# Kernel tuning notes

Measured on AMD Instinct MI355X. Metric: run time of the kernel, lower is better.

The kernel has to match this reference:

```python
import jax, jax.numpy as jnp
import numpy as np
import math

N_PTS = 262144
STEP_LENGTH = math.sqrt(3.0) / 1024.0  # step_length = sqrt(3)/steps


def pos_enc(x):
    # classic NeRF frequency encoding: identity + sin/cos at 10 octaves -> 3 + 3*2*10 = 63
    freqs = 2.0 ** jnp.arange(10, dtype=x.dtype)            # [10]
    xb = x[..., :, None] * freqs                            # [N,3,10]
    xb = xb.reshape(x.shape[0], -1)                         # [N,30]
    return jnp.concatenate([x, jnp.sin(xb), jnp.cos(xb)], axis=-1)  # [N,63]


def dir_enc(u):
    # 26-dim frequency encoding of (dir+1)/2 (color head input 283 = 256 + 26 + 1).
    # 13 sin/cos pairs: per-channel octaves 2^0..2^4, truncated to 13 frequencies.
    freqs = 2.0 ** jnp.arange(5, dtype=u.dtype)             # [5]
    z = (u[..., :, None] * freqs).reshape(u.shape[0], -1)[:, :13]  # [N,13]
    return jnp.concatenate([jnp.sin(z), jnp.cos(z)], axis=-1)      # [N,26]


def linear(x, w, b):
    return x @ w.T + b


def setup_inputs() -> dict:
    key = jax.random.key(0)
    ks = jax.random.split(key, 16)
    s = 0.05
    inp = {
        "position": jax.random.uniform(ks[0], (N_PTS, 3), dtype=jnp.float32),
        "direction": jax.random.uniform(ks[1], (N_PTS, 3), dtype=jnp.float32, minval=-1.0, maxval=1.0),
        "w1_in": jax.random.normal(ks[2], (256, 63), jnp.float32) * s,
        "b1_in": jnp.zeros((256,), jnp.float32),
        "w1_h": jax.random.normal(ks[3], (3, 256, 256), jnp.float32) * s,
        "b1_h": jnp.zeros((3, 256), jnp.float32),
        "w2_in": jax.random.normal(ks[4], (256, 319), jnp.float32) * s,
        "b2_in": jnp.zeros((256,), jnp.float32),
        "w2_h": jax.random.normal(ks[5], (3, 256, 256), jnp.float32) * s,
        "b2_h": jnp.zeros((3, 256), jnp.float32),
        # sigma head Linear(256,1)
        "w_sigma": jax.random.normal(ks[6], (1, 256), jnp.float32) * s,
        "b_sigma": jnp.zeros((1,), jnp.float32),
        # color head Linear(283,128) -> ReLU -> Linear(128,3)
        "w_c1": jax.random.normal(ks[7], (128, 283), jnp.float32) * s,
        "b_c1": jnp.zeros((128,), jnp.float32),
        "w_c2": jax.random.normal(ks[8], (3, 128), jnp.float32) * s,
        "b_c2": jnp.zeros((3,), jnp.float32),
    }
    return inp


def reference(position, direction,
              w1_in, b1_in, w1_h, b1_h,
              w2_in, b2_in, w2_h, b2_h,
              w_sigma, b_sigma, w_c1, b_c1, w_c2, b_c2):
    pe = pos_enc(position)                                  # [N,63]
    h = jax.nn.relu(linear(pe, w1_in, b1_in))               # [N,256]
    for i in range(3):
        h = jax.nn.relu(linear(h, w1_h[i], b1_h[i]))
    g = jax.nn.relu(linear(jnp.concatenate([h, pe], axis=-1), w2_in, b2_in))  # [N,256]
    for i in range(3):
        g = jax.nn.relu(linear(g, w2_h[i], b2_h[i]))
    sigma_raw = linear(g, w_sigma, b_sigma)                 # [N,1]
    # get_alpha: 1 - exp(-relu(sigma) * step_length)
    alphas = 1.0 - jnp.exp(-jax.nn.relu(sigma_raw) * STEP_LENGTH)             # [N,1]
    # get_rgb: shares base features; concat [256 | 26 | 1] = 283
    de = dir_enc((direction + 1.0) * 0.5)                   # [N,26]
    feats = jnp.concatenate([g, de, sigma_raw], axis=-1)    # [N,283]
    rgb = jax.nn.sigmoid(linear(jax.nn.relu(linear(feats, w_c1, b_c1)), w_c2, b_c2))  # [N,3]
    return (rgb, alphas)
```

## Files before the change

kernel.cpp:

```cpp
#include <hip/hip_runtime.h>
#include <hip/hip_bf16.h>

#define N_PTS 262144
#define STEP_LEN 0.0016914558667664818f

using f32x4 = __attribute__((ext_vector_type(4))) float;
using s8 = __attribute__((ext_vector_type(8))) short;

__device__ __forceinline__ float bf2f(short s) {
    union { unsigned int u; float f; } v;
    v.u = ((unsigned int)(unsigned short)s) << 16;
    return v.f;
}
__device__ __forceinline__ short f2bf(float f) {
    __hip_bfloat16 h = __float2bfloat16(f);
    return *reinterpret_cast<short*>(&h);
}

#define OFF_W1    0
#define OFF_L1H0  16384
#define OFF_W2    212992
#define OFF_L2H0  294912
#define OFF_C1G   491520
#define OFF_C1DE  524288
#define OFF_WSIG  528384
#define OFF_WC2   528640
#define WS_ELEMS  532480

__device__ __forceinline__ float hid_val(const float* __restrict__ W, int e) {
    int j = e & 7, lane = (e >> 3) & 63, nt = (e >> 9) & 15, ks = e >> 13;
    int n = nt * 16 + (lane & 15), hi = lane >> 4;
    int f = ks * 32 + ((j >> 2) << 4) + hi * 4 + (j & 3);
    return W[n * 256 + f];
}

__global__ void prep_weights(const float* __restrict__ w1_in,
                             const float* __restrict__ w1_h,
                             const float* __restrict__ w2_in,
                             const float* __restrict__ w2_h,
                             const float* __restrict__ w_c1,
                             const float* __restrict__ w_sigma,
                             const float* __restrict__ w_c2,
                             __hip_bfloat16* __restrict__ ws) {
    int i = blockIdx.x * blockDim.x + threadIdx.x;
    if (i >= WS_ELEMS) return;
    float v;
    if (i < OFF_L1H0) {
        int e = i;
        int j = e & 7, lane = (e >> 3) & 63, nt = (e >> 9) & 15, ks = e >> 13;
        int n = nt * 16 + (lane & 15), hi = lane >> 4;
        int f = ks * 32 + hi * 8 + j;
        v = (f < 63) ? w1_in[n * 63 + f] : 0.f;
    } else if (i < OFF_W2) {
        int e = i - OFF_L1H0; int sub = e >> 16; e &= 65535;
        v = hid_val(w1_h + sub * 65536, e);
    } else if (i < OFF_L2H0) {
        int e = i - OFF_W2;
        int j = e & 7, lane = (e >> 3) & 63, nt = (e >> 9) & 15, ks = e >> 13;
        int n = nt * 16 + (lane & 15), hi = lane >> 4;
        if (ks < 8) {
            int f = ks * 32 + ((j >> 2) << 4) + hi * 4 + (j & 3);
            v = w2_in[n * 319 + f];
        } else {
            int pf = (ks - 8) * 32 + hi * 8 + j;
            v = (pf < 63) ? w2_in[n * 319 + 256 + pf] : 0.f;
        }
    } else if (i < OFF_C1G) {
        int e = i - OFF_L2H0; int sub = e >> 16; e &= 65535;
        v = hid_val(w2_h + sub * 65536, e);
    } else if (i < OFF_C1DE) {
        int e = i - OFF_C1G;
        int j = e & 7, lane = (e >> 3) & 63, nt = (e >> 9) & 7, ks = e >> 12;
        int n = nt * 16 + (lane & 15), hi = lane >> 4;
        int f = ks * 32 + ((j >> 2) << 4) + hi * 4 + (j & 3);
        v = w_c1[n * 283 + f];
    } else if (i < OFF_WSIG) {
        int e = i - OFF_C1DE;
        int j = e & 7, lane = (e >> 3) & 63, nt = (e >> 9) & 7;
        int n = nt * 16 + (lane & 15), hi = lane >> 4;
        int k = 256 + hi * 8 + j;
        v = (k < 283) ? w_c1[n * 283 + k] : 0.f;
    } else if (i < OFF_WC2) {
        int e = i - OFF_WSIG;
        int j = e & 7, hi = (e >> 3) & 3, ks = e >> 5;
        int f = ks * 32 + ((j >> 2) << 4) + hi * 4 + (j & 3);
        v = w_sigma[f];
    } else if (i < 529024) {
        int e = i - OFF_WC2;
        int j = e & 7, hi = (e >> 3) & 3, ks = (e >> 5) & 3, ch = e >> 7;
        int f = ks * 32 + ((j >> 2) << 4) + hi * 4 + (j & 3);
        v = w_c2[ch * 128 + f];
    } else {
        v = 0.f;
    }
    ws[i] = __float2bfloat16(v);
}

__device__ __forceinline__ float enc3(int f, float x0, float x1, float x2) {
    if (f < 3) return (f == 0) ? x0 : ((f == 1) ? x1 : x2);
    if (f < 33) {
        int q = f - 3; int c = q / 10, o = q % 10;
        float xc = (c == 0) ? x0 : ((c == 1) ? x1 : x2);
        return __sinf(xc * (float)(1 << o));
    }
    if (f < 63) {
        int q = f - 33; int c = q / 10, o = q % 10;
        float xc = (c == 0) ? x0 : ((c == 1) ? x1 : x2);
        return __cosf(xc * (float)(1 << o));
    }
    return 0.f;
}

#define MFMA16 __builtin_amdgcn_mfma_f32_16x16x32_bf16

#define STAGE4(BYTEOFF, DBUF) do { \
    const char* _src = wsB + (long)(BYTEOFF) + wid * 4096 + lane * 16; \
    char* _dst = (DBUF) + wid * 4096; \
    __builtin_amdgcn_global_load_lds((const unsigned int*)(_src),        (unsigned int*)(_dst),        16, 0, 0); \
    __builtin_amdgcn_global_load_lds((const unsigned int*)(_src + 1024), (unsigned int*)(_dst + 1024), 16, 0, 0); \
    __builtin_amdgcn_global_load_lds((const unsigned int*)(_src + 2048), (unsigned int*)(_dst + 2048), 16, 0, 0); \
    __builtin_amdgcn_global_load_lds((const unsigned int*)(_src + 3072), (unsigned int*)(_dst + 3072), 16, 0, 0); \
} while (0)

#define WKSTEP(RDBUF, STGOFF, WRBUF, A0, A1, FIRSTV) do { \
    STAGE4(STGOFF, WRBUF); \
    __builtin_amdgcn_s_setprio(1); \
    _Pragma("unroll") \
    for (int nt = 0; nt < 16; ++nt) { \
        const s8 w = *(const s8*)((RDBUF) + nt * 1024 + lane * 16); \
        acc[nt][0] = MFMA16(w, (A0), (FIRSTV) ? Z : acc[nt][0], 0, 0, 0); \
        acc[nt][1] = MFMA16(w, (A1), (FIRSTV) ? Z : acc[nt][1], 0, 0, 0); \
    } \
    __builtin_amdgcn_s_setprio(0); \
} while (0)

#define KBAR4 do { asm volatile("s_waitcnt vmcnt(4)" ::: "memory"); \
                   __builtin_amdgcn_s_barrier(); } while (0)
#define KBAR0 do { asm volatile("s_waitcnt vmcnt(0)" ::: "memory"); \
                   __builtin_amdgcn_s_barrier(); } while (0)

#define CONVERTL(BOFF) do { \
    _Pragma("unroll") \
    for (int nt = 0; nt < 16; ++nt) { \
        const f32x4 b4 = *(const f32x4*)(biasL + (((BOFF) + nt * 16 + hi4) << 2)); \
        _Pragma("unroll") \
        for (int r = 0; r < 4; ++r) { \
            actA[nt >> 1][((nt & 1) << 2) | r] = f2bf(fmaxf(acc[nt][0][r] + b4[r], 0.f)); \
            actB[nt >> 1][((nt & 1) << 2) | r] = f2bf(fmaxf(acc[nt][1][r] + b4[r], 0.f)); \
        } } } while (0)

#define CKSTEP(RDBUF, KS, FIRSTV) do { \
    __builtin_amdgcn_s_setprio(1); \
    _Pragma("unroll") \
    for (int nt = 0; nt < 8; ++nt) { \
        const s8 w = *(const s8*)((RDBUF) + nt * 1024 + lane * 16); \
        acc[nt][0] = MFMA16(w, actA[KS], (FIRSTV) ? Z : acc[nt][0], 0, 0, 0); \
        acc[nt][1] = MFMA16(w, actB[KS], (FIRSTV) ? Z : acc[nt][1], 0, 0, 0); \
    } \
    _Pragma("unroll") \
    for (int nt = 0; nt < 8; ++nt) { \
        const s8 w = *(const s8*)((RDBUF) + 8192 + nt * 1024 + lane * 16); \
        acc[nt][0] = MFMA16(w, actA[(KS) + 1], acc[nt][0], 0, 0, 0); \
        acc[nt][1] = MFMA16(w, actB[(KS) + 1], acc[nt][1], 0, 0, 0); \
    } \
    __builtin_amdgcn_s_setprio(0); \
} while (0)

__global__ __launch_bounds__(256, 2) void nerf_fused(
    const float* __restrict__ pos, const float* __restrict__ dir,
    const __hip_bfloat16* __restrict__ ws,
    const float* __restrict__ b1_in, const float* __restrict__ b1_h,
    const float* __restrict__ b2_in, const float* __restrict__ b2_h,
    const float* __restrict__ b_sigma, const float* __restrict__ b_c1,
    const float* __restrict__ b_c2,
    float* __restrict__ out) {

    __shared__ __align__(16) char Lds[74240];
    char* const S0 = Lds;
    char* const S1 = Lds + 16384;
    char* const S2 = Lds + 32768;
    char* const S3 = Lds + 49152;
    char* const biasL = Lds + 65536;

    const int t = threadIdx.x;
    const int lane = t & 63;
    const int wid = t >> 6;
    const int hi = lane >> 4;
    const int col = lane & 15;
    const int hi4 = hi * 4;
    const int row0 = blockIdx.x * 128;
    const int gA = row0 + wid * 32 + col;
    const int gB = gA + 16;
    const char* wsB = (const char*)ws;

    for (int i = t; i < 2176; i += 256) {
        float v;
        if (i < 256) v = b1_in[i];
        else if (i < 1024) v = b1_h[i - 256];
        else if (i < 1280) v = b2_in[i - 1024];
        else if (i < 2048) v = b2_h[i - 1280];
        else v = b_c1[i - 2048];
        *(float*)(biasL + i * 4) = v;
    }

    s8 peA0, peA1, peB0, peB1;
    {
        float xa0 = pos[gA*3], xa1 = pos[gA*3+1], xa2 = pos[gA*3+2];
        float xb0 = pos[gB*3], xb1 = pos[gB*3+1], xb2 = pos[gB*3+2];
#pragma unroll
        for (int j = 0; j < 8; ++j) {
            int f0 = hi * 8 + j, f1 = 32 + hi * 8 + j;
            peA0[j] = f2bf(enc3(f0, xa0, xa1, xa2));
            peA1[j] = f2bf(enc3(f1, xa0, xa1, xa2));
            peB0[j] = f2bf(enc3(f0, xb0, xb1, xb2));
            peB1[j] = f2bf(enc3(f1, xb0, xb1, xb2));
        }
    }

    f32x4 acc[16][2];
    s8 actA[8], actB[8];
    const f32x4 Z = {0.f, 0.f, 0.f, 0.f};

    STAGE4(0L, S0);
    STAGE4(16384L, S1);
    asm volatile("s_waitcnt vmcnt(4) lgkmcnt(0)" ::: "memory");
    __builtin_amdgcn_s_barrier();

    WKSTEP(S0, 2L*16384, S2, peA0, peB0, 1); KBAR4;
    WKSTEP(S1, 3L*16384, S3, peA1, peB1, 0); CONVERTL(0); KBAR4;

#pragma unroll 1
    for (int l = 0; l < 3; ++l) {
        const long lb = 65536L + (long)l * 131072;
        const int bo = 256 + (l << 8);
        WKSTEP(S2, lb,            S0, actA[0], actB[0], 1); KBAR4;
        WKSTEP(S3, lb + 16384,    S1, actA[1], actB[1], 0); KBAR4;
        WKSTEP(S0, lb + 2*16384,  S2, actA[2], actB[2], 0); KBAR4;
        WKSTEP(S1, lb + 3*16384,  S3, actA[3], actB[3], 0); KBAR4;
        WKSTEP(S2, lb + 4*16384,  S0, actA[4], actB[4], 0); KBAR4;
        WKSTEP(S3, lb + 5*16384,  S1, actA[5], actB[5], 0); KBAR4;
        WKSTEP(S0, lb + 6*16384,  S2, actA[6], actB[6], 0); KBAR4;
        WKSTEP(S1, lb + 7*16384,  S3, actA[7], actB[7], 0); CONVERTL(bo); KBAR4;
    }

    WKSTEP(S2, 28L*16384, S0, actA[0], actB[0], 1); KBAR4;
    WKSTEP(S3, 29L*16384, S1, actA[1], actB[1], 0); KBAR4;
    WKSTEP(S0, 30L*16384, S2, actA[2], actB[2], 0); KBAR4;
    WKSTEP(S1, 31L*16384, S3, actA[3], actB[3], 0); KBAR4;
    WKSTEP(S2, 32L*16384, S0, actA[4], actB[4], 0); KBAR4;
    WKSTEP(S3, 33L*16384, S1, actA[5], actB[5], 0); KBAR4;
    WKSTEP(S0, 34L*16384, S2, actA[6], actB[6], 0); KBAR4;
    WKSTEP(S1, 35L*16384, S3, actA[7], actB[7], 0); KBAR4;
    WKSTEP(S2, 36L*16384, S0, peA0,    peB0,    0); KBAR4;
    WKSTEP(S3, 37L*16384, S1, peA1,    peB1,    0); CONVERTL(1024); KBAR4;

#pragma unroll 1
    for (int l = 0; l < 3; ++l) {
        const long lb = (long)(38 + (l << 3)) * 16384;
        const int bo = 1280 + (l << 8);
        WKSTEP(S0, lb,            S2, actA[0], actB[0], 1); KBAR4;
        WKSTEP(S1, lb + 16384,    S3, actA[1], actB[1], 0); KBAR4;
        WKSTEP(S2, lb + 2*16384,  S0, actA[2], actB[2], 0); KBAR4;
        WKSTEP(S3, lb + 3*16384,  S1, actA[3], actB[3], 0); KBAR4;
        WKSTEP(S0, lb + 4*16384,  S2, actA[4], actB[4], 0); KBAR4;
        WKSTEP(S1, lb + 5*16384,  S3, actA[5], actB[5], 0); KBAR4;
        WKSTEP(S2, lb + 6*16384,  S0, actA[6], actB[6], 0); KBAR4;
        WKSTEP(S3, lb + 7*16384,  S1, actA[7], actB[7], 0); CONVERTL(bo); KBAR4;
    }

    float alphaA, alphaB, srA, srB;
    {
        float sA = 0.f, sB = 0.f;
#pragma unroll
        for (int ks = 0; ks < 8; ++ks) {
            const s8 wv = *(const s8*)(wsB + (OFF_WSIG + ks * 32 + hi * 8) * 2);
#pragma unroll
            for (int j = 0; j < 8; ++j) {
                sA += bf2f(actA[ks][j]) * bf2f(wv[j]);
                sB += bf2f(actB[ks][j]) * bf2f(wv[j]);
            }
        }
        sA += __shfl_xor(sA, 16); sA += __shfl_xor(sA, 32);
        sB += __shfl_xor(sB, 16); sB += __shfl_xor(sB, 32);
        srA = sA + b_sigma[0]; srB = sB + b_sigma[0];
        alphaA = 1.f - __expf(-fmaxf(srA, 0.f) * STEP_LEN);
        alphaB = 1.f - __expf(-fmaxf(srB, 0.f) * STEP_LEN);
    }

    s8 deA, deB;
    {
        float uA0 = (dir[gA*3+0] + 1.f) * 0.5f;
        float uA1 = (dir[gA*3+1] + 1.f) * 0.5f;
        float uA2 = (dir[gA*3+2] + 1.f) * 0.5f;
        float uB0 = (dir[gB*3+0] + 1.f) * 0.5f;
        float uB1 = (dir[gB*3+1] + 1.f) * 0.5f;
        float uB2 = (dir[gB*3+2] + 1.f) * 0.5f;
#pragma unroll
        for (int j = 0; j < 8; ++j) {
            int d = hi * 8 + j;
            float vA, vB;
            if (d < 13) {
                int c = d / 5, o = d % 5; float s = (float)(1 << o);
                vA = __sinf(((c == 0) ? uA0 : (c == 1) ? uA1 : uA2) * s);
                vB = __sinf(((c == 0) ? uB0 : (c == 1) ? uB1 : uB2) * s);
            } else if (d < 26) {
                int q = d - 13; int c = q / 5, o = q % 5; float s = (float)(1 << o);
                vA = __cosf(((c == 0) ? uA0 : (c == 1) ? uA1 : uA2) * s);
                vB = __cosf(((c == 0) ? uB0 : (c == 1) ? uB1 : uB2) * s);
            } else if (d == 26) {
                vA = srA; vB = srB;
            } else {
                vA = 0.f; vB = 0.f;
            }
            deA[j] = f2bf(vA); deB[j] = f2bf(vB);
        }
    }

    STAGE4(62L*16384, S2); CKSTEP(S0, 0, 1); KBAR4;
    STAGE4(63L*16384, S3); CKSTEP(S1, 2, 0); KBAR4;
    STAGE4(64L*16384, S0); CKSTEP(S2, 4, 0); KBAR4;
    CKSTEP(S3, 6, 0); KBAR0;
    {
        __builtin_amdgcn_s_setprio(1);
#pragma unroll
        for (int nt = 0; nt < 8; ++nt) {
            const s8 w = *(const s8*)(S0 + nt * 1024 + lane * 16);
            acc[nt][0] = MFMA16(w, deA, acc[nt][0], 0, 0, 0);
            acc[nt][1] = MFMA16(w, deB, acc[nt][1], 0, 0, 0);
        }
        __builtin_amdgcn_s_setprio(0);
    }

    s8 c1A[4], c1B[4];
#pragma unroll
    for (int nt = 0; nt < 8; ++nt) {
        const f32x4 b4 = *(const f32x4*)(biasL + ((2048 + nt * 16 + hi4) << 2));
#pragma unroll
        for (int r = 0; r < 4; ++r) {
            c1A[nt >> 1][((nt & 1) << 2) | r] = f2bf(fmaxf(acc[nt][0][r] + b4[r], 0.f));
            c1B[nt >> 1][((nt & 1) << 2) | r] = f2bf(fmaxf(acc[nt][1][r] + b4[r], 0.f));
        }
    }

#pragma unroll
    for (int ch = 0; ch < 3; ++ch) {
        float rA = 0.f, rB = 0.f;
#pragma unroll
        for (int ks = 0; ks < 4; ++ks) {
            const s8 wv = *(const s8*)(wsB + (OFF_WC2 + (ch * 4 + ks) * 32 + hi * 8) * 2);
#pragma unroll
            for (int j = 0; j < 8; ++j) {
                rA += bf2f(c1A[ks][j]) * bf2f(wv[j]);
                rB += bf2f(c1B[ks][j]) * bf2f(wv[j]);
            }
        }
        rA += __shfl_xor(rA, 16); rA += __shfl_xor(rA, 32);
        rB += __shfl_xor(rB, 16); rB += __shfl_xor(rB, 32);
        if (hi == 0) {
            out[gA * 3 + ch] = 1.f / (1.f + __expf(-(rA + b_c2[ch])));
            out[gB * 3 + ch] = 1.f / (1.f + __expf(-(rB + b_c2[ch])));
        }
    }
    if (hi == 0) {
        out[3 * N_PTS + gA] = alphaA;
        out[3 * N_PTS + gB] = alphaB;
    }
}

extern "C" void kernel_launch(void* const* d_in, const int* in_sizes, int n_in,
                              void* d_out, int out_size, void* d_ws, size_t ws_size,
                              hipStream_t stream) {
    const float* position = (const float*)d_in[0];
    const float* direction = (const float*)d_in[1];
    const float* w1_in = (const float*)d_in[2];
    const float* b1_in = (const float*)d_in[3];
    const float* w1_h  = (const float*)d_in[4];
    const float* b1_h  = (const float*)d_in[5];
    const float* w2_in = (const float*)d_in[6];
    const float* b2_in = (const float*)d_in[7];
    const float* w2_h  = (const float*)d_in[8];
    const float* b2_h  = (const float*)d_in[9];
    const float* w_sigma = (const float*)d_in[10];
    const float* b_sigma = (const float*)d_in[11];
    const float* w_c1  = (const float*)d_in[12];
    const float* b_c1  = (const float*)d_in[13];
    const float* w_c2  = (const float*)d_in[14];
    const float* b_c2  = (const float*)d_in[15];
    float* out = (float*)d_out;
    __hip_bfloat16* ws = (__hip_bfloat16*)d_ws;

    prep_weights<<<(WS_ELEMS + 255) / 256, 256, 0, stream>>>(
        w1_in, w1_h, w2_in, w2_h, w_c1, w_sigma, w_c2, ws);

    nerf_fused<<<N_PTS / 128, 256, 0, stream>>>(
        position, direction, ws,
        b1_in, b1_h, b2_in, b2_h,
        b_sigma, b_c1, b_c2, out);
}
```

Measured before the change: 240.3 us.

## Double per-wave row tile to 64 points to halve weight traffic per point

Each wave now processes four 16-row subtiles (64 points) instead of two, so every weight fragment read from LDS feeds four MFMAs. Blocks cover 256 points and the grid is halved. Accumulators grow to 16x4 f32x4, so launch bounds drop to 1 block per CU and the positional encoding is recomputed instead of kept live. The intent is to cut weight staging and LDS reads per point, at the cost of lower occupancy and heavy register pressure that may cause spills.

```diff
diff --git a/kernel.cpp b/kernel.cpp
--- a/kernel.cpp
+++ b/kernel.cpp
@@ -122,14 +122,28 @@
     __builtin_amdgcn_global_load_lds((const unsigned int*)(_src + 3072), (unsigned int*)(_dst + 3072), 16, 0, 0); \
 } while (0)
 
-#define WKSTEP(RDBUF, STGOFF, WRBUF, A0, A1, FIRSTV) do { \
+#define WKSTEP_A(RDBUF, STGOFF, WRBUF, KS, FIRSTV) do { \
     STAGE4(STGOFF, WRBUF); \
     __builtin_amdgcn_s_setprio(1); \
     _Pragma("unroll") \
     for (int nt = 0; nt < 16; ++nt) { \
         const s8 w = *(const s8*)((RDBUF) + nt * 1024 + lane * 16); \
-        acc[nt][0] = MFMA16(w, (A0), (FIRSTV) ? Z : acc[nt][0], 0, 0, 0); \
-        acc[nt][1] = MFMA16(w, (A1), (FIRSTV) ? Z : acc[nt][1], 0, 0, 0); \
+        _Pragma("unroll") \
+        for (int s = 0; s < 4; ++s) \
+            acc[nt][s] = MFMA16(w, act[KS][s], (FIRSTV) ? Z : acc[nt][s], 0, 0, 0); \
+    } \
+    __builtin_amdgcn_s_setprio(0); \
+} while (0)
+
+#define WKSTEP_P(RDBUF, STGOFF, WRBUF, PEV, FIRSTV) do { \
+    STAGE4(STGOFF, WRBUF); \
+    __builtin_amdgcn_s_setprio(1); \
+    _Pragma("unroll") \
+    for (int nt = 0; nt < 16; ++nt) { \
+        const s8 w = *(const s8*)((RDBUF) + nt * 1024 + lane * 16); \
+        _Pragma("unroll") \
+        for (int s = 0; s < 4; ++s) \
+            acc[nt][s] = MFMA16(w, PEV[s], (FIRSTV) ? Z : acc[nt][s], 0, 0, 0); \
     } \
     __builtin_amdgcn_s_setprio(0); \
 } while (0)
@@ -144,9 +158,10 @@
     for (int nt = 0; nt < 16; ++nt) { \
         const f32x4 b4 = *(const f32x4*)(biasL + (((BOFF) + nt * 16 + hi4) << 2)); \
         _Pragma("unroll") \
-        for (int r = 0; r < 4; ++r) { \
-            actA[nt >> 1][((nt & 1) << 2) | r] = f2bf(fmaxf(acc[nt][0][r] + b4[r], 0.f)); \
-            actB[nt >> 1][((nt & 1) << 2) | r] = f2bf(fmaxf(acc[nt][1][r] + b4[r], 0.f)); \
+        for (int s = 0; s < 4; ++s) { \
+            _Pragma("unroll") \
+            for (int r = 0; r < 4; ++r) \
+                act[nt >> 1][s][((nt & 1) << 2) | r] = f2bf(fmaxf(acc[nt][s][r] + b4[r], 0.f)); \
         } } } while (0)
 
 #define CKSTEP(RDBUF, KS, FIRSTV) do { \
@@ -154,19 +169,21 @@
     _Pragma("unroll") \
     for (int nt = 0; nt < 8; ++nt) { \
         const s8 w = *(const s8*)((RDBUF) + nt * 1024 + lane * 16); \
-        acc[nt][0] = MFMA16(w, actA[KS], (FIRSTV) ? Z : acc[nt][0], 0, 0, 0); \
-        acc[nt][1] = MFMA16(w, actB[KS], (FIRSTV) ? Z : acc[nt][1], 0, 0, 0); \
+        _Pragma("unroll") \
+        for (int s = 0; s < 4; ++s) \
+            acc[nt][s] = MFMA16(w, act[KS][s], (FIRSTV) ? Z : acc[nt][s], 0, 0, 0); \
     } \
     _Pragma("unroll") \
     for (int nt = 0; nt < 8; ++nt) { \
         const s8 w = *(const s8*)((RDBUF) + 8192 + nt * 1024 + lane * 16); \
-        acc[nt][0] = MFMA16(w, actA[(KS) + 1], acc[nt][0], 0, 0, 0); \
-        acc[nt][1] = MFMA16(w, actB[(KS) + 1], acc[nt][1], 0, 0, 0); \
+        _Pragma("unroll") \
+        for (int s = 0; s < 4; ++s) \
+            acc[nt][s] = MFMA16(w, act[(KS) + 1][s], acc[nt][s], 0, 0, 0); \
     } \
     __builtin_amdgcn_s_setprio(0); \
 } while (0)
 
-__global__ __launch_bounds__(256, 2) void nerf_fused(
+__global__ __launch_bounds__(256, 1) void nerf_fused(
     const float* __restrict__ pos, const float* __restrict__ dir,
     const __hip_bfloat16* __restrict__ ws,
     const float* __restrict__ b1_in, const float* __restrict__ b1_h,
@@ -188,9 +205,7 @@
     const int hi = lane >> 4;
     const int col = lane & 15;
     const int hi4 = hi * 4;
-    const int row0 = blockIdx.x * 128;
-    const int gA = row0 + wid * 32 + col;
-    const int gB = gA + 16;
+    const int base = blockIdx.x * 256 + wid * 64 + col;
     const char* wsB = (const char*)ws;
 
     for (int i = t; i < 2176; i += 256) {
@@ -203,22 +218,23 @@
         *(float*)(biasL + i * 4) = v;
     }
 
-    s8 peA0, peA1, peB0, peB1;
-    {
-        float xa0 = pos[gA*3], xa1 = pos[gA*3+1], xa2 = pos[gA*3+2];
-        float xb0 = pos[gB*3], xb1 = pos[gB*3+1], xb2 = pos[gB*3+2];
-#pragma unroll
-        for (int j = 0; j < 8; ++j) {
-            int f0 = hi * 8 + j, f1 = 32 + hi * 8 + j;
-            peA0[j] = f2bf(enc3(f0, xa0, xa1, xa2));
-            peA1[j] = f2bf(enc3(f1, xa0, xa1, xa2));
-            peB0[j] = f2bf(enc3(f0, xb0, xb1, xb2));
-            peB1[j] = f2bf(enc3(f1, xb0, xb1, xb2));
-        }
-    }
-
-    f32x4 acc[16][2];
-    s8 actA[8], actB[8];
+    s8 pe0[4], pe1[4];
+    auto make_pe = [&]() {
+#pragma unroll
+        for (int s = 0; s < 4; ++s) {
+            int g = base + s * 16;
+            float x0 = pos[g*3], x1 = pos[g*3+1], x2 = pos[g*3+2];
+#pragma unroll
+            for (int j = 0; j < 8; ++j) {
+                pe0[s][j] = f2bf(enc3(hi * 8 + j, x0, x1, x2));
+                pe1[s][j] = f2bf(enc3(32 + hi * 8 + j, x0, x1, x2));
+            }
+        }
+    };
+    make_pe();
+
+    f32x4 acc[16][4];
+    s8 act[8][4];
     const f32x4 Z = {0.f, 0.f, 0.f, 0.f};
 
     STAGE4(0L, S0);
@@ -226,93 +242,95 @@
     asm volatile("s_waitcnt vmcnt(4) lgkmcnt(0)" ::: "memory");
     __builtin_amdgcn_s_barrier();
 
-    WKSTEP(S0, 2L*16384, S2, peA0, peB0, 1); KBAR4;
-    WKSTEP(S1, 3L*16384, S3, peA1, peB1, 0); CONVERTL(0); KBAR4;
+    WKSTEP_P(S0, 2L*16384, S2, pe0, 1); KBAR4;
+    WKSTEP_P(S1, 3L*16384, S3, pe1, 0); CONVERTL(0); KBAR4;
 
 #pragma unroll 1
     for (int l = 0; l < 3; ++l) {
         const long lb = 65536L + (long)l * 131072;
         const int bo = 256 + (l << 8);
-        WKSTEP(S2, lb,            S0, actA[0], actB[0], 1); KBAR4;
-        WKSTEP(S3, lb + 16384,    S1, actA[1], actB[1], 0); KBAR4;
-        WKSTEP(S0, lb + 2*16384,  S2, actA[2], actB[2], 0); KBAR4;
-        WKSTEP(S1, lb + 3*16384,  S3, actA[3], actB[3], 0); KBAR4;
-        WKSTEP(S2, lb + 4*16384,  S0, actA[4], actB[4], 0); KBAR4;
-        WKSTEP(S3, lb + 5*16384,  S1, actA[5], actB[5], 0); KBAR4;
-        WKSTEP(S0, lb + 6*16384,  S2, actA[6], actB[6], 0); KBAR4;
-        WKSTEP(S1, lb + 7*16384,  S3, actA[7], actB[7], 0); CONVERTL(bo); KBAR4;
-    }
-
-    WKSTEP(S2, 28L*16384, S0, actA[0], actB[0], 1); KBAR4;
-    WKSTEP(S3, 29L*16384, S1, actA[1], actB[1], 0); KBAR4;
-    WKSTEP(S0, 30L*16384, S2, actA[2], actB[2], 0); KBAR4;
-    WKSTEP(S1, 31L*16384, S3, actA[3], actB[3], 0); KBAR4;
-    WKSTEP(S2, 32L*16384, S0, actA[4], actB[4], 0); KBAR4;
-    WKSTEP(S3, 33L*16384, S1, actA[5], actB[5], 0); KBAR4;
-    WKSTEP(S0, 34L*16384, S2, actA[6], actB[6], 0); KBAR4;
-    WKSTEP(S1, 35L*16384, S3, actA[7], actB[7], 0); KBAR4;
-    WKSTEP(S2, 36L*16384, S0, peA0,    peB0,    0); KBAR4;
-    WKSTEP(S3, 37L*16384, S1, peA1,    peB1,    0); CONVERTL(1024); KBAR4;
+        WKSTEP_A(S2, lb,            S0, 0, 1); KBAR4;
+        WKSTEP_A(S3, lb + 16384,    S1, 1, 0); KBAR4;
+        WKSTEP_A(S0, lb + 2*16384,  S2, 2, 0); KBAR4;
+        WKSTEP_A(S1, lb + 3*16384,  S3, 3, 0); KBAR4;
+        WKSTEP_A(S2, lb + 4*16384,  S0, 4, 0); KBAR4;
+        WKSTEP_A(S3, lb + 5*16384,  S1, 5, 0); KBAR4;
+        WKSTEP_A(S0, lb + 6*16384,  S2, 6, 0); KBAR4;
+        WKSTEP_A(S1, lb + 7*16384,  S3, 7, 0); CONVERTL(bo); KBAR4;
+    }
+
+    make_pe();
+
+    WKSTEP_A(S2, 28L*16384, S0, 0, 1); KBAR4;
+    WKSTEP_A(S3, 29L*16384, S1, 1, 0); KBAR4;
+    WKSTEP_A(S0, 30L*16384, S2, 2, 0); KBAR4;
+    WKSTEP_A(S1, 31L*16384, S3, 3, 0); KBAR4;
+    WKSTEP_A(S2, 32L*16384, S0, 4, 0); KBAR4;
+    WKSTEP_A(S3, 33L*16384, S1, 5, 0); KBAR4;
+    WKSTEP_A(S0, 34L*16384, S2, 6, 0); KBAR4;
+    WKSTEP_A(S1, 35L*16384, S3, 7, 0); KBAR4;
+    WKSTEP_P(S2, 36L*16384, S0, pe0, 0); KBAR4;
+    WKSTEP_P(S3, 37L*16384, S1, pe1, 0); CONVERTL(1024); KBAR4;
 
 #pragma unroll 1
     for (int l = 0; l < 3; ++l) {
         const long lb = (long)(38 + (l << 3)) * 16384;
         const int bo = 1280 + (l << 8);
-        WKSTEP(S0, lb,            S2, actA[0], actB[0], 1); KBAR4;
-        WKSTEP(S1, lb + 16384,    S3, actA[1], actB[1], 0); KBAR4;
-        WKSTEP(S2, lb + 2*16384,  S0, actA[2], actB[2], 0); KBAR4;
-        WKSTEP(S3, lb + 3*16384,  S1, actA[3], actB[3], 0); KBAR4;
-        WKSTEP(S0, lb + 4*16384,  S2, actA[4], actB[4], 0); KBAR4;
-        WKSTEP(S1, lb + 5*16384,  S3, actA[5], actB[5], 0); KBAR4;
-        WKSTEP(S2, lb + 6*16384,  S0, actA[6], actB[6], 0); KBAR4;
-        WKSTEP(S3, lb + 7*16384,  S1, actA[7], actB[7], 0); CONVERTL(bo); KBAR4;
-    }
-
-    float alphaA, alphaB, srA, srB;
+        WKSTEP_A(S0, lb,            S2, 0, 1); KBAR4;
+        WKSTEP_A(S1, lb + 16384,    S3, 1, 0); KBAR4;
+        WKSTEP_A(S2, lb + 2*16384,  S0, 2, 0); KBAR4;
+        WKSTEP_A(S3, lb + 3*16384,  S1, 3, 0); KBAR4;
+        WKSTEP_A(S0, lb + 4*16384,  S2, 4, 0); KBAR4;
+        WKSTEP_A(S1, lb + 5*16384,  S3, 5, 0); KBAR4;
+        WKSTEP_A(S2, lb + 6*16384,  S0, 6, 0); KBAR4;
+        WKSTEP_A(S3, lb + 7*16384,  S1, 7, 0); CONVERTL(bo); KBAR4;
+    }
+
+    float sr[4], alpha[4];
     {
-        float sA = 0.f, sB = 0.f;
+        float sm[4] = {0.f, 0.f, 0.f, 0.f};
 #pragma unroll
         for (int ks = 0; ks < 8; ++ks) {
             const s8 wv = *(const s8*)(wsB + (OFF_WSIG + ks * 32 + hi * 8) * 2);
 #pragma unroll
-            for (int j = 0; j < 8; ++j) {
-                sA += bf2f(actA[ks][j]) * bf2f(wv[j]);
-                sB += bf2f(actB[ks][j]) * bf2f(wv[j]);
+            for (int s = 0; s < 4; ++s) {
+#pragma unroll
+                for (int j = 0; j < 8; ++j)
+                    sm[s] += bf2f(act[ks][s][j]) * bf2f(wv[j]);
             }
         }
-        sA += __shfl_xor(sA, 16); sA += __shfl_xor(sA, 32);
-        sB += __shfl_xor(sB, 16); sB += __shfl_xor(sB, 32);
-        srA = sA + b_sigma[0]; srB = sB + b_sigma[0];
-        alphaA = 1.f - __expf(-fmaxf(srA, 0.f) * STEP_LEN);
-        alphaB = 1.f - __expf(-fmaxf(srB, 0.f) * STEP_LEN);
-    }
-
-    s8 deA, deB;
-    {
-        float uA0 = (dir[gA*3+0] + 1.f) * 0.5f;
-        float uA1 = (dir[gA*3+1] + 1.f) * 0.5f;
-        float uA2 = (dir[gA*3+2] + 1.f) * 0.5f;
-        float uB0 = (dir[gB*3+0] + 1.f) * 0.5f;
-        float uB1 = (dir[gB*3+1] + 1.f) * 0.5f;
-        float uB2 = (dir[gB*3+2] + 1.f) * 0.5f;
+#pragma unroll
+        for (int s = 0; s < 4; ++s) {
+            sm[s] += __shfl_xor(sm[s], 16);
+            sm[s] += __shfl_xor(sm[s], 32);
+            sr[s] = sm[s] + b_sigma[0];
+            alpha[s] = 1.f - __expf(-fmaxf(sr[s], 0.f) * STEP_LEN);
+        }
+    }
+
+    s8 de[4];
+#pragma unroll
+    for (int s = 0; s < 4; ++s) {
+        int g = base + s * 16;
+        float u0 = (dir[g*3+0] + 1.f) * 0.5f;
+        float u1 = (dir[g*3+1] + 1.f) * 0.5f;
+        float u2 = (dir[g*3+2] + 1.f) * 0.5f;
 #pragma unroll
         for (int j = 0; j < 8; ++j) {
             int d = hi * 8 + j;
-            float vA, vB;
+            float v;
             if (d < 13) {
-                int c = d / 5, o = d % 5; float s = (float)(1 << o);
-                vA = __sinf(((c == 0) ? uA0 : (c == 1) ? uA1 : uA2) * s);
-                vB = __sinf(((c == 0) ? uB0 : (c == 1) ? uB1 : uB2) * s);
+                int c = d / 5, o = d % 5;
+                v = __sinf(((c == 0) ? u0 : (c == 1) ? u1 : u2) * (float)(1 << o));
             } else if (d < 26) {
-                int q = d - 13; int c = q / 5, o = q % 5; float s = (float)(1 << o);
-                vA = __cosf(((c == 0) ? uA0 : (c == 1) ? uA1 : uA2) * s);
-                vB = __cosf(((c == 0) ? uB0 : (c == 1) ? uB1 : uB2) * s);
+                int q = d - 13; int c = q / 5, o = q % 5;
+                v = __cosf(((c == 0) ? u0 : (c == 1) ? u1 : u2) * (float)(1 << o));
             } else if (d == 26) {
-                vA = srA; vB = srB;
+                v = sr[s];
             } else {
-                vA = 0.f; vB = 0.f;
+                v = 0.f;
             }
-            deA[j] = f2bf(vA); deB[j] = f2bf(vB);
+            de[s][j] = f2bf(v);
         }
     }
 
@@ -325,45 +343,50 @@
 #pragma unroll
         for (int nt = 0; nt < 8; ++nt) {
             const s8 w = *(const s8*)(S0 + nt * 1024 + lane * 16);
-            acc[nt][0] = MFMA16(w, deA, acc[nt][0], 0, 0, 0);
-            acc[nt][1] = MFMA16(w, deB, acc[nt][1], 0, 0, 0);
+#pragma unroll
+            for (int s = 0; s < 4; ++s)
+                acc[nt][s] = MFMA16(w, de[s], acc[nt][s], 0, 0, 0);
         }
         __builtin_amdgcn_s_setprio(0);
     }
 
-    s8 c1A[4], c1B[4];
+    s8 c1[4][4];
 #pragma unroll
     for (int nt = 0; nt < 8; ++nt) {
         const f32x4 b4 = *(const f32x4*)(biasL + ((2048 + nt * 16 + hi4) << 2));
 #pragma unroll
-        for (int r = 0; r < 4; ++r) {
-            c1A[nt >> 1][((nt & 1) << 2) | r] = f2bf(fmaxf(acc[nt][0][r] + b4[r], 0.f));
-            c1B[nt >> 1][((nt & 1) << 2) | r] = f2bf(fmaxf(acc[nt][1][r] + b4[r], 0.f));
+        for (int s = 0; s < 4; ++s) {
+#pragma unroll
+            for (int r = 0; r < 4; ++r)
+                c1[nt >> 1][s][((nt & 1) << 2) | r] = f2bf(fmaxf(acc[nt][s][r] + b4[r], 0.f));
         }
     }
 
 #pragma unroll
     for (int ch = 0; ch < 3; ++ch) {
-        float rA = 0.f, rB = 0.f;
+        float rr[4] = {0.f, 0.f, 0.f, 0.f};
 #pragma unroll
         for (int ks = 0; ks < 4; ++ks) {
             const s8 wv = *(const s8*)(wsB + (OFF_WC2 + (ch * 4 + ks) * 32 + hi * 8) * 2);
 #pragma unroll
-            for (int j = 0; j < 8; ++j) {
-                rA += bf2f(c1A[ks][j]) * bf2f(wv[j]);
-                rB += bf2f(c1B[ks][j]) * bf2f(wv[j]);
+            for (int s = 0; s < 4; ++s) {
+#pragma unroll
+                for (int j = 0; j < 8; ++j)
+                    rr[s] += bf2f(c1[ks][s][j]) * bf2f(wv[j]);
             }
         }
-        rA += __shfl_xor(rA, 16); rA += __shfl_xor(rA, 32);
-        rB += __shfl_xor(rB, 16); rB += __shfl_xor(rB, 32);
-        if (hi == 0) {
-            out[gA * 3 + ch] = 1.f / (1.f + __expf(-(rA + b_c2[ch])));
-            out[gB * 3 + ch] = 1.f / (1.f + __expf(-(rB + b_c2[ch])));
+#pragma unroll
+        for (int s = 0; s < 4; ++s) {
+            rr[s] += __shfl_xor(rr[s], 16);
+            rr[s] += __shfl_xor(rr[s], 32);
+            if (hi == 0)
+                out[(base + s * 16) * 3 + ch] = 1.f / (1.f + __expf(-(rr[s] + b_c2[ch])));
         }
     }
     if (hi == 0) {
-        out[3 * N_PTS + gA] = alphaA;
-        out[3 * N_PTS + gB] = alphaB;
+#pragma unroll
+        for (int s = 0; s < 4; ++s)
+            out[3 * N_PTS + base + s * 16] = alpha[s];
     }
 }
 
@@ -392,7 +415,7 @@
     prep_weights<<<(WS_ELEMS + 255) / 256, 256, 0, stream>>>(
         w1_in, w1_h, w2_in, w2_h, w_c1, w_sigma, w_c2, ws);
 
-    nerf_fused<<<N_PTS / 128, 256, 0, stream>>>(
+    nerf_fused<<<N_PTS / 256, 256, 0, stream>>>(
         position, direction, ws,
         b1_in, b1_h, b2_in, b2_h,
         b_sigma, b_c1, b_c2, out);
```

Measured after the change: 401.1 us. 66.9% more time.

## Stage three quarters of weight tiles via LDS, load last quarter directly to registers

Applied to the files above, without the earlier changes.

Each 16 KB weight chunk is now split so that 12 KB is staged into LDS with global_load_lds and the remaining 4 KB is read by each wave straight from global memory into registers for the last four output tiles. This shrinks the LDS footprint from about 74 KB to 58 KB, which could allow more blocks per CU and reduces LDS traffic. Positional encoding is now computed on demand into a single register pair instead of being held live throughout, lowering register pressure. The trade-off is redundant per-wave global (L2) reads of the direct-loaded portion and more outstanding vector memory operations that must complete before use.

```diff
diff --git a/kernel.cpp b/kernel.cpp
--- a/kernel.cpp
+++ b/kernel.cpp
@@ -113,28 +113,103 @@
 
 #define MFMA16 __builtin_amdgcn_mfma_f32_16x16x32_bf16
 
-#define STAGE4(BYTEOFF, DBUF) do { \
-    const char* _src = wsB + (long)(BYTEOFF) + wid * 4096 + lane * 16; \
-    char* _dst = (DBUF) + wid * 4096; \
-    __builtin_amdgcn_global_load_lds((const unsigned int*)(_src),        (unsigned int*)(_dst),        16, 0, 0); \
-    __builtin_amdgcn_global_load_lds((const unsigned int*)(_src + 1024), (unsigned int*)(_dst + 1024), 16, 0, 0); \
-    __builtin_amdgcn_global_load_lds((const unsigned int*)(_src + 2048), (unsigned int*)(_dst + 2048), 16, 0, 0); \
-    __builtin_amdgcn_global_load_lds((const unsigned int*)(_src + 3072), (unsigned int*)(_dst + 3072), 16, 0, 0); \
+#define GLL(SRC, DST) __builtin_amdgcn_global_load_lds( \
+    (const unsigned int*)(SRC), (unsigned int*)(DST), 16, 0, 0)
+
+#define STAGE3(BYTEOFF, DBUF) do { \
+    const char* _src = wsB + (long)(BYTEOFF) + wid * 3072 + lane * 16; \
+    char* _dst = (DBUF) + wid * 3072; \
+    GLL(_src, _dst); \
+    GLL(_src + 1024, _dst + 1024); \
+    GLL(_src + 2048, _dst + 2048); \
 } while (0)
 
-#define WKSTEP(RDBUF, STGOFF, WRBUF, A0, A1, FIRSTV) do { \
-    STAGE4(STGOFF, WRBUF); \
+#define DLOAD(CUROFF) \
+    const char* _dp = wsB + (long)(CUROFF) + 12288 + lane * 16; \
+    const s8 d0 = *(const s8*)(_dp); \
+    const s8 d1 = *(const s8*)(_dp + 1024); \
+    const s8 d2 = *(const s8*)(_dp + 2048); \
+    const s8 d3 = *(const s8*)(_dp + 3072); \
+    __builtin_amdgcn_sched_barrier(0)
+
+#define WK12_A(RDBUF, CUROFF, STGOFF, WRBUF, KS, FIRSTV) do { \
+    DLOAD(CUROFF); \
+    STAGE3(STGOFF, WRBUF); \
     __builtin_amdgcn_s_setprio(1); \
     _Pragma("unroll") \
-    for (int nt = 0; nt < 16; ++nt) { \
+    for (int nt = 0; nt < 12; ++nt) { \
         const s8 w = *(const s8*)((RDBUF) + nt * 1024 + lane * 16); \
-        acc[nt][0] = MFMA16(w, (A0), (FIRSTV) ? Z : acc[nt][0], 0, 0, 0); \
-        acc[nt][1] = MFMA16(w, (A1), (FIRSTV) ? Z : acc[nt][1], 0, 0, 0); \
+        acc[nt][0] = MFMA16(w, act[KS][0], (FIRSTV) ? Z : acc[nt][0], 0, 0, 0); \
+        acc[nt][1] = MFMA16(w, act[KS][1], (FIRSTV) ? Z : acc[nt][1], 0, 0, 0); \
     } \
+    acc[12][0] = MFMA16(d0, act[KS][0], (FIRSTV) ? Z : acc[12][0], 0, 0, 0); \
+    acc[12][1] = MFMA16(d0, act[KS][1], (FIRSTV) ? Z : acc[12][1], 0, 0, 0); \
+    acc[13][0] = MFMA16(d1, act[KS][0], (FIRSTV) ? Z : acc[13][0], 0, 0, 0); \
+    acc[13][1] = MFMA16(d1, act[KS][1], (FIRSTV) ? Z : acc[13][1], 0, 0, 0); \
+    acc[14][0] = MFMA16(d2, act[KS][0], (FIRSTV) ? Z : acc[14][0], 0, 0, 0); \
+    acc[14][1] = MFMA16(d2, act[KS][1], (FIRSTV) ? Z : acc[14][1], 0, 0, 0); \
+    acc[15][0] = MFMA16(d3, act[KS][0], (FIRSTV) ? Z : acc[15][0], 0, 0, 0); \
+    acc[15][1] = MFMA16(d3, act[KS][1], (FIRSTV) ? Z : acc[15][1], 0, 0, 0); \
     __builtin_amdgcn_s_setprio(0); \
 } while (0)
 
-#define KBAR4 do { asm volatile("s_waitcnt vmcnt(4)" ::: "memory"); \
+#define WK12_P(RDBUF, CUROFF, STGOFF, WRBUF, FIRSTV) do { \
+    DLOAD(CUROFF); \
+    STAGE3(STGOFF, WRBUF); \
+    __builtin_amdgcn_s_setprio(1); \
+    _Pragma("unroll") \
+    for (int nt = 0; nt < 12; ++nt) { \
+        const s8 w = *(const s8*)((RDBUF) + nt * 1024 + lane * 16); \
+        acc[nt][0] = MFMA16(w, peC[0], (FIRSTV) ? Z : acc[nt][0], 0, 0, 0); \
+        acc[nt][1] = MFMA16(w, peC[1], (FIRSTV) ? Z : acc[nt][1], 0, 0, 0); \
+    } \
+    acc[12][0] = MFMA16(d0, peC[0], (FIRSTV) ? Z : acc[12][0], 0, 0, 0); \
+    acc[12][1] = MFMA16(d0, peC[1], (FIRSTV) ? Z : acc[12][1], 0, 0, 0); \
+    acc[13][0] = MFMA16(d1, peC[0], (FIRSTV) ? Z : acc[13][0], 0, 0, 0); \
+    acc[13][1] = MFMA16(d1, peC[1], (FIRSTV) ? Z : acc[13][1], 0, 0, 0); \
+    acc[14][0] = MFMA16(d2, peC[0], (FIRSTV) ? Z : acc[14][0], 0, 0, 0); \
+    acc[14][1] = MFMA16(d2, peC[1], (FIRSTV) ? Z : acc[14][1], 0, 0, 0); \
+    acc[15][0] = MFMA16(d3, peC[0], (FIRSTV) ? Z : acc[15][0], 0, 0, 0); \
+    acc[15][1] = MFMA16(d3, peC[1], (FIRSTV) ? Z : acc[15][1], 0, 0, 0); \
+    __builtin_amdgcn_s_setprio(0); \
+} while (0)
+
+#define CK12_BODY(RDBUF, KS, FIRSTV) \
+    __builtin_amdgcn_s_setprio(1); \
+    _Pragma("unroll") \
+    for (int nt = 0; nt < 8; ++nt) { \
+        const s8 w = *(const s8*)((RDBUF) + nt * 1024 + lane * 16); \
+        acc[nt][0] = MFMA16(w, act[KS][0], (FIRSTV) ? Z : acc[nt][0], 0, 0, 0); \
+        acc[nt][1] = MFMA16(w, act[KS][1], (FIRSTV) ? Z : acc[nt][1], 0, 0, 0); \
+    } \
+    _Pragma("unroll") \
+    for (int nt = 0; nt < 4; ++nt) { \
+        const s8 w = *(const s8*)((RDBUF) + 8192 + nt * 1024 + lane * 16); \
+        acc[nt][0] = MFMA16(w, act[(KS) + 1][0], acc[nt][0], 0, 0, 0); \
+        acc[nt][1] = MFMA16(w, act[(KS) + 1][1], acc[nt][1], 0, 0, 0); \
+    } \
+    acc[4][0] = MFMA16(d0, act[(KS) + 1][0], acc[4][0], 0, 0, 0); \
+    acc[4][1] = MFMA16(d0, act[(KS) + 1][1], acc[4][1], 0, 0, 0); \
+    acc[5][0] = MFMA16(d1, act[(KS) + 1][0], acc[5][0], 0, 0, 0); \
+    acc[5][1] = MFMA16(d1, act[(KS) + 1][1], acc[5][1], 0, 0, 0); \
+    acc[6][0] = MFMA16(d2, act[(KS) + 1][0], acc[6][0], 0, 0, 0); \
+    acc[6][1] = MFMA16(d2, act[(KS) + 1][1], acc[6][1], 0, 0, 0); \
+    acc[7][0] = MFMA16(d3, act[(KS) + 1][0], acc[7][0], 0, 0, 0); \
+    acc[7][1] = MFMA16(d3, act[(KS) + 1][1], acc[7][1], 0, 0, 0); \
+    __builtin_amdgcn_s_setprio(0)
+
+#define CK12S(RDBUF, CUROFF, STGOFF, WRBUF, KS, FIRSTV) do { \
+    DLOAD(CUROFF); \
+    STAGE3(STGOFF, WRBUF); \
+    CK12_BODY(RDBUF, KS, FIRSTV); \
+} while (0)
+
+#define CK12N(RDBUF, CUROFF, KS, FIRSTV) do { \
+    DLOAD(CUROFF); \
+    CK12_BODY(RDBUF, KS, FIRSTV); \
+} while (0)
+
+#define KBAR3 do { asm volatile("s_waitcnt vmcnt(3)" ::: "memory"); \
                    __builtin_amdgcn_s_barrier(); } while (0)
 #define KBAR0 do { asm volatile("s_waitcnt vmcnt(0)" ::: "memory"); \
                    __builtin_amdgcn_s_barrier(); } while (0)
@@ -145,26 +220,9 @@
         const f32x4 b4 = *(const f32x4*)(biasL + (((BOFF) + nt * 16 + hi4) << 2)); \
         _Pragma("unroll") \
         for (int r = 0; r < 4; ++r) { \
-            actA[nt >> 1][((nt & 1) << 2) | r] = f2bf(fmaxf(acc[nt][0][r] + b4[r], 0.f)); \
-            actB[nt >> 1][((nt & 1) << 2) | r] = f2bf(fmaxf(acc[nt][1][r] + b4[r], 0.f)); \
+            act[nt >> 1][0][((nt & 1) << 2) | r] = f2bf(fmaxf(acc[nt][0][r] + b4[r], 0.f)); \
+            act[nt >> 1][1][((nt & 1) << 2) | r] = f2bf(fmaxf(acc[nt][1][r] + b4[r], 0.f)); \
         } } } while (0)
-
-#define CKSTEP(RDBUF, KS, FIRSTV) do { \
-    __builtin_amdgcn_s_setprio(1); \
-    _Pragma("unroll") \
-    for (int nt = 0; nt < 8; ++nt) { \
-        const s8 w = *(const s8*)((RDBUF) + nt * 1024 + lane * 16); \
-        acc[nt][0] = MFMA16(w, actA[KS], (FIRSTV) ? Z : acc[nt][0], 0, 0, 0); \
-        acc[nt][1] = MFMA16(w, actB[KS], (FIRSTV) ? Z : acc[nt][1], 0, 0, 0); \
-    } \
-    _Pragma("unroll") \
-    for (int nt = 0; nt < 8; ++nt) { \
-        const s8 w = *(const s8*)((RDBUF) + 8192 + nt * 1024 + lane * 16); \
-        acc[nt][0] = MFMA16(w, actA[(KS) + 1], acc[nt][0], 0, 0, 0); \
-        acc[nt][1] = MFMA16(w, actB[(KS) + 1], acc[nt][1], 0, 0, 0); \
-    } \
-    __builtin_amdgcn_s_setprio(0); \
-} while (0)
 
 __global__ __launch_bounds__(256, 2) void nerf_fused(
     const float* __restrict__ pos, const float* __restrict__ dir,
@@ -175,12 +233,12 @@
     const float* __restrict__ b_c2,
     float* __restrict__ out) {
 
-    __shared__ __align__(16) char Lds[74240];
+    __shared__ __align__(16) char Lds[57856];
     char* const S0 = Lds;
-    char* const S1 = Lds + 16384;
-    char* const S2 = Lds + 32768;
-    char* const S3 = Lds + 49152;
-    char* const biasL = Lds + 65536;
+    char* const S1 = Lds + 12288;
+    char* const S2 = Lds + 24576;
+    char* const S3 = Lds + 36864;
+    char* const biasL = Lds + 49152;
 
     const int t = threadIdx.x;
     const int lane = t & 63;
@@ -203,72 +261,74 @@
         *(float*)(biasL + i * 4) = v;
     }
 
-    s8 peA0, peA1, peB0, peB1;
-    {
-        float xa0 = pos[gA*3], xa1 = pos[gA*3+1], xa2 = pos[gA*3+2];
-        float xb0 = pos[gB*3], xb1 = pos[gB*3+1], xb2 = pos[gB*3+2];
+    const float pxA = pos[gA*3], pyA = pos[gA*3+1], pzA = pos[gA*3+2];
+    const float pxB = pos[gB*3], pyB = pos[gB*3+1], pzB = pos[gB*3+2];
+    s8 peC[2];
+    auto make_pe = [&](int half) {
 #pragma unroll
         for (int j = 0; j < 8; ++j) {
-            int f0 = hi * 8 + j, f1 = 32 + hi * 8 + j;
-            peA0[j] = f2bf(enc3(f0, xa0, xa1, xa2));
-            peA1[j] = f2bf(enc3(f1, xa0, xa1, xa2));
-            peB0[j] = f2bf(enc3(f0, xb0, xb1, xb2));
-            peB1[j] = f2bf(enc3(f1, xb0, xb1, xb2));
-        }
-    }
+            int f = half * 32 + hi * 8 + j;
+            peC[0][j] = f2bf(enc3(f, pxA, pyA, pzA));
+            peC[1][j] = f2bf(enc3(f, pxB, pyB, pzB));
+        }
+    };
+    make_pe(0);
 
     f32x4 acc[16][2];
-    s8 actA[8], actB[8];
+    s8 act[8][2];
     const f32x4 Z = {0.f, 0.f, 0.f, 0.f};
 
-    STAGE4(0L, S0);
-    STAGE4(16384L, S1);
-    asm volatile("s_waitcnt vmcnt(4) lgkmcnt(0)" ::: "memory");
+    STAGE3(0L, S0);
+    STAGE3(16384L, S1);
+    asm volatile("s_waitcnt vmcnt(3) lgkmcnt(0)" ::: "memory");
     __builtin_amdgcn_s_barrier();
 
-    WKSTEP(S0, 2L*16384, S2, peA0, peB0, 1); KBAR4;
-    WKSTEP(S1, 3L*16384, S3, peA1, peB1, 0); CONVERTL(0); KBAR4;
+    WK12_P(S0, 0L,     2L*16384, S2, 1); KBAR3;
+    make_pe(1);
+    WK12_P(S1, 16384L, 3L*16384, S3, 0); CONVERTL(0); KBAR3;
 
 #pragma unroll 1
     for (int l = 0; l < 3; ++l) {
-        const long lb = 65536L + (long)l * 131072;
+        const long cb = 32768L + (long)l * 131072;
         const int bo = 256 + (l << 8);
-        WKSTEP(S2, lb,            S0, actA[0], actB[0], 1); KBAR4;
-        WKSTEP(S3, lb + 16384,    S1, actA[1], actB[1], 0); KBAR4;
-        WKSTEP(S0, lb + 2*16384,  S2, actA[2], actB[2], 0); KBAR4;
-        WKSTEP(S1, lb + 3*16384,  S3, actA[3], actB[3], 0); KBAR4;
-        WKSTEP(S2, lb + 4*16384,  S0, actA[4], actB[4], 0); KBAR4;
-        WKSTEP(S3, lb + 5*16384,  S1, actA[5], actB[5], 0); KBAR4;
-        WKSTEP(S0, lb + 6*16384,  S2, actA[6], actB[6], 0); KBAR4;
-        WKSTEP(S1, lb + 7*16384,  S3, actA[7], actB[7], 0); CONVERTL(bo); KBAR4;
-    }
-
-    WKSTEP(S2, 28L*16384, S0, actA[0], actB[0], 1); KBAR4;
-    WKSTEP(S3, 29L*16384, S1, actA[1], actB[1], 0); KBAR4;
-    WKSTEP(S0, 30L*16384, S2, actA[2], actB[2], 0); KBAR4;
-    WKSTEP(S1, 31L*16384, S3, actA[3], actB[3], 0); KBAR4;
-    WKSTEP(S2, 32L*16384, S0, actA[4], actB[4], 0); KBAR4;
-    WKSTEP(S3, 33L*16384, S1, actA[5], actB[5], 0); KBAR4;
-    WKSTEP(S0, 34L*16384, S2, actA[6], actB[6], 0); KBAR4;
-    WKSTEP(S1, 35L*16384, S3, actA[7], actB[7], 0); KBAR4;
-    WKSTEP(S2, 36L*16384, S0, peA0,    peB0,    0); KBAR4;
-    WKSTEP(S3, 37L*16384, S1, peA1,    peB1,    0); CONVERTL(1024); KBAR4;
+        WK12_A(S2, cb,            cb + 2*16384, S0, 0, 1); KBAR3;
+        WK12_A(S3, cb +   16384,  cb + 3*16384, S1, 1, 0); KBAR3;
+        WK12_A(S0, cb + 2*16384,  cb + 4*16384, S2, 2, 0); KBAR3;
+        WK12_A(S1, cb + 3*16384,  cb + 5*16384, S3, 3, 0); KBAR3;
+        WK12_A(S2, cb + 4*16384,  cb + 6*16384, S0, 4, 0); KBAR3;
+        WK12_A(S3, cb + 5*16384,  cb + 7*16384, S1, 5, 0); KBAR3;
+        WK12_A(S0, cb + 6*16384,  cb + 8*16384, S2, 6, 0); KBAR3;
+        WK12_A(S1, cb + 7*16384,  cb + 9*16384, S3, 7, 0); CONVERTL(bo); KBAR3;
+    }
+
+    WK12_A(S2, 26L*16384, 28L*16384, S0, 0, 1); KBAR3;
+    WK12_A(S3, 27L*16384, 29L*16384, S1, 1, 0); KBAR3;
+    WK12_A(S0, 28L*16384, 30L*16384, S2, 2, 0); KBAR3;
+    WK12_A(S1, 29L*16384, 31L*16384, S3, 3, 0); KBAR3;
+    WK12_A(S2, 30L*16384, 32L*16384, S0, 4, 0); KBAR3;
+    WK12_A(S3, 31L*16384, 33L*16384, S1, 5, 0); KBAR3;
+    WK12_A(S0, 32L*16384, 34L*16384, S2, 6, 0); KBAR3;
+    WK12_A(S1, 33L*16384, 35L*16384, S3, 7, 0); KBAR3;
+    make_pe(0);
+    WK12_P(S2, 34L*16384, 36L*16384, S0, 0); KBAR3;
+    make_pe(1);
+    WK12_P(S3, 35L*16384, 37L*16384, S1, 0); CONVERTL(1024); KBAR3;
 
 #pragma unroll 1
     for (int l = 0; l < 3; ++l) {
-        const long lb = (long)(38 + (l << 3)) * 16384;
+        const long cb = (long)(36 + (l << 3)) * 16384;
         const int bo = 1280 + (l << 8);
-        WKSTEP(S0, lb,            S2, actA[0], actB[0], 1); KBAR4;
-        WKSTEP(S1, lb + 16384,    S3, actA[1], actB[1], 0); KBAR4;
-        WKSTEP(S2, lb + 2*16384,  S0, actA[2], actB[2], 0); KBAR4;
-        WKSTEP(S3, lb + 3*16384,  S1, actA[3], actB[3], 0); KBAR4;
-        WKSTEP(S0, lb + 4*16384,  S2, actA[4], actB[4], 0); KBAR4;
-        WKSTEP(S1, lb + 5*16384,  S3, actA[5], actB[5], 0); KBAR4;
-        WKSTEP(S2, lb + 6*16384,  S0, actA[6], actB[6], 0); KBAR4;
-        WKSTEP(S3, lb + 7*16384,  S1, actA[7], actB[7], 0); CONVERTL(bo); KBAR4;
-    }
-
-    float alphaA, alphaB, srA, srB;
+        WK12_A(S0, cb,            cb + 2*16384, S2, 0, 1); KBAR3;
+        WK12_A(S1, cb +   16384,  cb + 3*16384, S3, 1, 0); KBAR3;
+        WK12_A(S2, cb + 2*16384,  cb + 4*16384, S0, 2, 0); KBAR3;
+        WK12_A(S3, cb + 3*16384,  cb + 5*16384, S1, 3, 0); KBAR3;
+        WK12_A(S0, cb + 4*16384,  cb + 6*16384, S2, 4, 0); KBAR3;
+        WK12_A(S1, cb + 5*16384,  cb + 7*16384, S3, 5, 0); KBAR3;
+        WK12_A(S2, cb + 6*16384,  cb + 8*16384, S0, 6, 0); KBAR3;
+        WK12_A(S3, cb + 7*16384,  cb + 9*16384, S1, 7, 0); CONVERTL(bo); KBAR3;
+    }
+
+    float srA, srB, alphaA, alphaB;
     {
         float sA = 0.f, sB = 0.f;
 #pragma unroll
@@ -276,8 +336,8 @@
             const s8 wv = *(const s8*)(wsB + (OFF_WSIG + ks * 32 + hi * 8) * 2);
 #pragma unroll
             for (int j = 0; j < 8; ++j) {
-                sA += bf2f(actA[ks][j]) * bf2f(wv[j]);
-                sB += bf2f(actB[ks][j]) * bf2f(wv[j]);
+                sA += bf2f(act[ks][0][j]) * bf2f(wv[j]);
+                sB += bf2f(act[ks][1][j]) * bf2f(wv[j]);
             }
         }
         sA += __shfl_xor(sA, 16); sA += __shfl_xor(sA, 32);
@@ -316,10 +376,10 @@
         }
     }
 
-    STAGE4(62L*16384, S2); CKSTEP(S0, 0, 1); KBAR4;
-    STAGE4(63L*16384, S3); CKSTEP(S1, 2, 0); KBAR4;
-    STAGE4(64L*16384, S0); CKSTEP(S2, 4, 0); KBAR4;
-    CKSTEP(S3, 6, 0); KBAR0;
+    CK12S(S0, 60L*16384, 62L*16384, S2, 0, 1); KBAR3;
+    CK12S(S1, 61L*16384, 63L*16384, S3, 2, 0); KBAR3;
+    CK12S(S2, 62L*16384, 64L*16384, S0, 4, 0); KBAR3;
+    CK12N(S3, 63L*16384, 6, 0); KBAR0;
     {
         __builtin_amdgcn_s_setprio(1);
 #pragma unroll
```

Measured after the change: 275.0 us. 14.4% more time.
